# Optimization experiments

Hardware: AMD Instinct MI355X
Metric: run time of the kernel (lower is better)

The kernel has to match this reference:

```python
import jax, jax.numpy as jnp
import numpy as np
from jax import lax

DN = ('NCDHW', 'OIDHW', 'NCDHW')
BN_EPS = 1e-5  # eval-mode BatchNorm3d with running_mean=0, running_var=1


def conv3d(x, w, b):
    y = lax.conv_general_dilated(x, w, window_strides=(1, 1, 1),
                                 padding=[(1, 1)] * 3, dimension_numbers=DN)
    return y + b[None, :, None, None, None]


def maxpool2(x):
    return lax.reduce_window(x, -jnp.inf, lax.max,
                             (1, 1, 2, 2, 2), (1, 1, 2, 2, 2), 'VALID')


def spline_block(x, cw, cb, knots, sw, w1, w2, g, beta):
    # SplineConv3d: conv -> (BSpline3D blend with SiLU) -> BN(eval) -> maxpool
    y = conv3d(x, cw, cb)                                   # [b,c,d,h,w]
    basis = jnp.maximum(y[..., None] - knots, 0.0) ** 3     # [b,c,d,h,w,k]
    sp = jnp.einsum('bcdhwk,ck->bcdhw', basis, sw)
    out = (w1[None, :, None, None, None] * sp
           + w2[None, :, None, None, None] * (y * jax.nn.sigmoid(y)))
    scale = (g / jnp.sqrt(1.0 + BN_EPS))[None, :, None, None, None]
    return maxpool2(out * scale + beta[None, :, None, None, None])


def setup_inputs() -> dict:
    key = jax.random.key(0)
    ks = iter(jax.random.split(key, 40))
    def nrm(shape, s=1.0):
        return jax.random.normal(next(ks), shape, dtype=jnp.float32) * s
    d = {}
    d['x'] = nrm((2, 1, 64, 64, 64))
    for cin, cout, t in [(1, 32, '1'), (32, 64, '2'), (64, 128, '3')]:
        d[f'c{t}_w'] = nrm((cout, cin, 3, 3, 3), 0.1)
        d[f'c{t}_b'] = nrm((cout,), 0.01)
        d[f'c{t}_knots'] = jnp.linspace(-1.0, 1.0, 10).astype(jnp.float32)
        d[f'c{t}_sw'] = nrm((cout, 10), 0.2)
        d[f'c{t}_w1'] = nrm((cout,), 0.2)
        d[f'c{t}_w2'] = nrm((cout,), 0.2)
        d[f'bn{t}_g'] = 1.0 + nrm((cout,), 0.1)
        d[f'bn{t}_b'] = nrm((cout,), 0.1)
    d['fc1_w'] = nrm((256, 128), 0.05)
    d['fc1_b'] = nrm((256,), 0.01)
    d['fc2_w'] = nrm((2, 256), 0.05)
    d['fc2_b'] = nrm((2,), 0.01)
    return d


def reference(x,
              c1_w, c1_b, c1_knots, c1_sw, c1_w1, c1_w2, bn1_g, bn1_b,
              c2_w, c2_b, c2_knots, c2_sw, c2_w1, c2_w2, bn2_g, bn2_b,
              c3_w, c3_b, c3_knots, c3_sw, c3_w1, c3_w2, bn3_g, bn3_b,
              fc1_w, fc1_b, fc2_w, fc2_b):
    h = spline_block(x, c1_w, c1_b, c1_knots, c1_sw, c1_w1, c1_w2, bn1_g, bn1_b)
    h = spline_block(h, c2_w, c2_b, c2_knots, c2_sw, c2_w1, c2_w2, bn2_g, bn2_b)
    h = spline_block(h, c3_w, c3_b, c3_knots, c3_sw, c3_w1, c3_w2, bn3_g, bn3_b)
    h = h.mean(axis=(2, 3, 4))          # AdaptiveAvgPool3d((1,1,1)) + flatten
    h = jax.nn.relu(h @ fc1_w.T + fc1_b)  # dropout is identity in eval mode
    return h @ fc2_w.T + fc2_b
```

## Files before the change

kernel.cpp:

```cpp
#include <hip/hip_runtime.h>
#include <math.h>


#define GLOBAL_AS __attribute__((address_space(1)))
#define LDS_AS    __attribute__((address_space(3)))

static __device__ __forceinline__ void async_ld16(const float* g, float* l) {
    __builtin_amdgcn_global_load_lds((const GLOBAL_AS void*)g, (LDS_AS void*)l,
                                     16, 0, 0);
}

template <int TPB_, int CIN, int CSPLIT, int G,
          int WDT, int WHT, int WWT, int BD, int BH, int BW>
__global__ __launch_bounds__(TPB_, 2) void spline_block_kernel(
    const float* __restrict__ x,
    const float* __restrict__ cw,
    const float* __restrict__ cb,
    const float* __restrict__ knots,
    const float* __restrict__ sw,
    const float* __restrict__ w1,
    const float* __restrict__ w2,
    const float* __restrict__ g,
    const float* __restrict__ beta,
    const float* __restrict__ zbuf,
    float* __restrict__ out,
    int N, int Cout, int D, int H, int W,
    int ntiles, int nthw, int ntw)
{
    constexpr int NSW    = BD * BH * BW;
    constexpr int NW     = TPB_ / 64;
    constexpr int CPG    = CIN / CSPLIT;
    constexpr int ID     = 2 * WDT + 2;
    constexpr int IH     = 2 * WHT + 2;
    constexpr int CHK    = (WWT + 4) / 2;
    constexpr int PITCH  = CHK * 4;
    constexpr int ROWS   = ID * IH;
    constexpr int CHUNKS = ROWS * CHK;
    constexpr int PHYS   = CHUNKS * 4;
    constexpr int NCH    = (CHUNKS + 63) / 64;
    constexpr int BUFS   = (CPG > 1) ? 2 : 1;
    static_assert(NW == NSW * CSPLIT, "waves = spatial-tiles x cin-split");
    static_assert(WDT * WHT * WWT == 64, "one wave per spatial tile");
    static_assert(CIN % CSPLIT == 0, "cin divisible");
    static_assert(NCH <= 32, "mask fits u32");
    static_assert(NCH == 6, "s_waitcnt vmcnt(6) literal assumes 6 issues/cin");
    static_assert(CSPLIT == 1 ||
                  (CSPLIT - 1) * 64 * G * 8 <= NW * BUFS * PHYS,
                  "reduction scratch fits in tile");

    __shared__ __align__(16) float tile[NW][BUFS][PHYS];
    __shared__ float  wlds[CIN * G * 28];
    __shared__ float4 stbl[G * 11];

    const int PD = D >> 1, PH = H >> 1, PW = W >> 1;
    const int groups = Cout / G;
    const int tid  = threadIdx.x;
    const int wv   = tid >> 6;
    const int lane = tid & 63;
    const int sw_  = wv % NSW;
    const int cg   = wv / NSW;

    const int bx      = blockIdx.x;
    const int tile_id = bx % ntiles;
    const int t1      = bx / ntiles;
    const int grp     = t1 % groups;
    const int n       = t1 / groups;
    const int c0      = grp * G;
    const int cinbase = cg * CPG;

    const int td  = tile_id / nthw;
    const int rem = tile_id % nthw;
    const int th_ = rem / ntw;
    const int tw_ = rem % ntw;

    for (int i = tid; i < CIN * G * 27; i += TPB_) {
        const int t  = i % 27;
        const int cgr = i / 27;
        const int gg = cgr % G;
        const int ci = cgr / G;
        wlds[cgr * 28 + t] = cw[((c0 + gg) * CIN + ci) * 27 + t];
    }
    for (int i = tid; i < G * 11; i += TPB_) {
        const int gg  = i / 11;
        const int cnt = i % 11;
        const int c   = c0 + gg;
        float A = 0.f, B3 = 0.f, C3 = 0.f, Dd = 0.f;
        for (int j = 0; j < cnt; j++) {
            const float s = sw[c * 10 + j];
            const float k = knots[j];
            A  += s;
            B3 += 3.0f * s * k;
            C3 += 3.0f * s * k * k;
            Dd += s * k * k * k;
        }
        stbl[i] = make_float4(A, B3, C3, Dd);
    }

    const int swd = sw_ / (BH * BW);
    const int r2  = sw_ % (BH * BW);
    const int swh = r2 / BW;
    const int sww = r2 % BW;
    const int pd0 = td  * (BD * WDT) + swd * WDT;
    const int ph0 = th_ * (BH * WHT) + swh * WHT;
    const int pw0 = tw_ * (BW * WWT) + sww * WWT;

    const int pwl = lane % WWT;
    const int phl = (lane / WWT) % WHT;
    const int pdl = lane / (WWT * WHT);

    const int d0 = 2 * pd0 - 1, h0 = 2 * ph0 - 1;
    const int w0 = 2 * pw0 - 1;
    const int wb = w0 & ~3;
    const int woff = w0 - wb;

    int off[NCH];
    unsigned vm = 0;
#pragma unroll
    for (int k = 0; k < NCH; k++) {
        const int chunk = lane + 64 * k;
        const int row = chunk / CHK, cs = chunk - row * CHK;
        const int dz = row / IH, hy = row - dz * IH;
        const int dd = d0 + dz, hh = h0 + hy;
        const int wsd = wb + cs * 4;
        const bool ok = (chunk < CHUNKS) &
                        ((unsigned)dd < (unsigned)D) &
                        ((unsigned)hh < (unsigned)H) &
                        ((unsigned)wsd < (unsigned)W);
        off[k] = ok ? (dd * H + hh) * W + wsd : 0;
        vm |= (unsigned)ok << k;
    }

    const size_t chstride = (size_t)D * H * W;
    const float* xn = x + (size_t)n * CIN * chstride;

    float acc[G][8];
#pragma unroll
    for (int gg = 0; gg < G; gg++)
#pragma unroll
        for (int i = 0; i < 8; i++) acc[gg][i] = 0.0f;

    __syncthreads();

    auto stage = [&](int ci, int buf) {
        const float* xc = xn + (size_t)ci * chstride;
        float* dst = &tile[wv][buf][0];
#pragma unroll
        for (int k = 0; k < NCH; k++) {
            const int chunk = lane + 64 * k;
            if ((k + 1) * 64 <= CHUNKS || chunk < CHUNKS) {
                const float* src = ((vm >> k) & 1) ? (xc + off[k]) : zbuf;
                async_ld16(src, dst + chunk * 4);
            }
        }
    };

    stage(cinbase, 0);

#pragma unroll 1
    for (int s = 0; s < CPG; s++) {
        const int cur = s & (BUFS - 1);
        if (s + 1 < CPG) {
            stage(cinbase + s + 1, cur ^ 1);
            asm volatile("s_waitcnt vmcnt(6)" ::: "memory");
        } else {
            asm volatile("s_waitcnt vmcnt(0)" ::: "memory");
        }

        const int ci = cinbase + s;
        const float* tb = &tile[wv][cur][0];
        float r[64];
#pragma unroll
        for (int dz = 0; dz < 4; dz++)
#pragma unroll
        for (int dy = 0; dy < 4; dy++) {
            const int rb = ((2 * pdl + dz) * IH + (2 * phl + dy)) * PITCH +
                           woff + 2 * pwl;
            r[(dz * 4 + dy) * 4 + 0] = tb[rb + 0];
            r[(dz * 4 + dy) * 4 + 1] = tb[rb + 1];
            r[(dz * 4 + dy) * 4 + 2] = tb[rb + 2];
            r[(dz * 4 + dy) * 4 + 3] = tb[rb + 3];
        }

#pragma unroll
        for (int gg = 0; gg < G; gg++) {
            const float4* w4p = (const float4*)&wlds[(ci * G + gg) * 28];
#pragma unroll
            for (int ch = 0; ch < 7; ch++) {
                const float4 wv4 = w4p[ch];
#pragma unroll
                for (int j = 0; j < 4; j++) {
                    const int tap = ch * 4 + j;
                    if (tap < 27) {
                        const float wvj = (j == 0) ? wv4.x : (j == 1) ? wv4.y
                                        : (j == 2) ? wv4.z : wv4.w;
                        const int kd = tap / 9, kh = (tap % 9) / 3, kw = tap % 3;
#pragma unroll
                        for (int od = 0; od < 2; od++)
#pragma unroll
                        for (int oh = 0; oh < 2; oh++)
#pragma unroll
                        for (int ow = 0; ow < 2; ow++)
                            acc[gg][(od * 2 + oh) * 2 + ow] =
                                fmaf(wvj,
                                     r[((od + kd) * 4 + (oh + kh)) * 4 + (ow + kw)],
                                     acc[gg][(od * 2 + oh) * 2 + ow]);
                    }
                }
            }
        }
    }

    float* af = &acc[0][0];
    if (CSPLIT > 1) {
        __syncthreads();
        float* scratch = &tile[0][0][0];
        if (cg > 0) {
#pragma unroll
            for (int idx = 0; idx < G * 8; idx++)
                scratch[(idx * (CSPLIT - 1) + (cg - 1)) * 64 + lane] = af[idx];
        }
        __syncthreads();
        if (cg == 0) {
#pragma unroll
            for (int idx = 0; idx < G * 8; idx++) {
                float s2 = af[idx];
                for (int j = 0; j < CSPLIT - 1; j++)
                    s2 += scratch[(idx * (CSPLIT - 1) + j) * 64 + lane];
                af[idx] = s2;
            }
        }
    }

    if (cg == 0) {
        const int pdg = pd0 + pdl, phg = ph0 + phl, pwg = pw0 + pwl;
#pragma unroll
        for (int gg = 0; gg < G; gg++) {
            const int c = c0 + gg;
            const float bias = cb[c];
            const float W1 = w1[c], W2 = w2[c];
            const float scale = g[c] * rsqrtf(1.0f + 1e-5f);
            const float bb = beta[c];

            float m = -INFINITY;
#pragma unroll
            for (int i = 0; i < 8; i++) {
                const float y = acc[gg][i] + bias;
                int idx = (int)floorf((y + 1.0f) * 4.5f) + 1;
                idx = min(max(idx, 0), 10);
                const float4 cf = stbl[gg * 11 + idx];
                const float sp = ((cf.x * y - cf.y) * y + cf.z) * y - cf.w;
                const float silu = y / (1.0f + __expf(-y));
                const float o = fmaf(W1 * sp + W2 * silu, scale, bb);
                m = fmaxf(m, o);
            }
            out[((size_t)(n * Cout + c) * PD + pdg) * PH * PW + phg * PW + pwg] = m;
        }
    }
}

__global__ __launch_bounds__(64) void mean_kernel(
    const float* __restrict__ h, float* __restrict__ out, int S)
{
    const int nc = blockIdx.x;
    const int lane = threadIdx.x;
    const float* p = h + (size_t)nc * S;
    float s = 0.0f;
    for (int i = lane; i < S; i += 64) s += p[i];
#pragma unroll
    for (int off = 32; off > 0; off >>= 1) s += __shfl_down(s, off, 64);
    if (lane == 0) out[nc] = s / (float)S;
}

__global__ __launch_bounds__(256) void fc_kernel(
    const float* __restrict__ pooled,
    const float* __restrict__ w1, const float* __restrict__ b1,
    const float* __restrict__ w2, const float* __restrict__ b2,
    float* __restrict__ out)
{
    __shared__ float hbuf[2][256];
    const int j = threadIdx.x;
#pragma unroll
    for (int nn = 0; nn < 2; nn++) {
        float s = b1[j];
        for (int k = 0; k < 128; k++)
            s = fmaf(pooled[nn * 128 + k], w1[j * 128 + k], s);
        hbuf[nn][j] = fmaxf(s, 0.0f);
    }
    __syncthreads();
    const int wid = j >> 6, lane = j & 63;
    const int nn = wid >> 1, oo = wid & 1;
    float s = 0.0f;
    for (int k = lane; k < 256; k += 64) s += hbuf[nn][k] * w2[oo * 256 + k];
#pragma unroll
    for (int off = 32; off > 0; off >>= 1) s += __shfl_down(s, off, 64);
    if (lane == 0) out[nn * 2 + oo] = s + b2[oo];
}

extern "C" void kernel_launch(void* const* d_in, const int* in_sizes, int n_in,
                              void* d_out, int out_size, void* d_ws, size_t ws_size,
                              hipStream_t stream) {
    const float* x      = (const float*)d_in[0];
    const float* c1_w   = (const float*)d_in[1];
    const float* c1_b   = (const float*)d_in[2];
    const float* c1_kn  = (const float*)d_in[3];
    const float* c1_sw  = (const float*)d_in[4];
    const float* c1_w1  = (const float*)d_in[5];
    const float* c1_w2  = (const float*)d_in[6];
    const float* bn1_g  = (const float*)d_in[7];
    const float* bn1_b  = (const float*)d_in[8];
    const float* c2_w   = (const float*)d_in[9];
    const float* c2_b   = (const float*)d_in[10];
    const float* c2_kn  = (const float*)d_in[11];
    const float* c2_sw  = (const float*)d_in[12];
    const float* c2_w1  = (const float*)d_in[13];
    const float* c2_w2  = (const float*)d_in[14];
    const float* bn2_g  = (const float*)d_in[15];
    const float* bn2_b  = (const float*)d_in[16];
    const float* c3_w   = (const float*)d_in[17];
    const float* c3_b   = (const float*)d_in[18];
    const float* c3_kn  = (const float*)d_in[19];
    const float* c3_sw  = (const float*)d_in[20];
    const float* c3_w1  = (const float*)d_in[21];
    const float* c3_w2  = (const float*)d_in[22];
    const float* bn3_g  = (const float*)d_in[23];
    const float* bn3_b  = (const float*)d_in[24];
    const float* fc1_w  = (const float*)d_in[25];
    const float* fc1_b  = (const float*)d_in[26];
    const float* fc2_w  = (const float*)d_in[27];
    const float* fc2_b  = (const float*)d_in[28];

    float* ws = (float*)d_ws;
    float* h1     = ws;
    float* h2     = h1 + 2097152;
    float* h3     = h2 + 524288;
    float* pooled = h3 + 131072;
    float* zbuf   = pooled + 256;

    hipMemsetAsync(zbuf, 0, 64, stream);

    spline_block_kernel<256, 1, 1, 4, 2, 4, 8, 2, 2, 1>
        <<<dim3(2048), dim3(256), 0, stream>>>(
        x, c1_w, c1_b, c1_kn, c1_sw, c1_w1, c1_w2, bn1_g, bn1_b, zbuf, h1,
        2, 32, 64, 64, 64, 128, 16, 4);
    spline_block_kernel<256, 32, 1, 4, 2, 4, 8, 2, 2, 1>
        <<<dim3(512), dim3(256), 0, stream>>>(
        h1, c2_w, c2_b, c2_kn, c2_sw, c2_w1, c2_w2, bn2_g, bn2_b, zbuf, h2,
        2, 64, 32, 32, 32, 16, 4, 2);
    spline_block_kernel<256, 64, 4, 4, 2, 4, 8, 1, 1, 1>
        <<<dim3(512), dim3(256), 0, stream>>>(
        h2, c3_w, c3_b, c3_kn, c3_sw, c3_w1, c3_w2, bn3_g, bn3_b, zbuf, h3,
        2, 128, 16, 16, 16, 8, 2, 1);
    mean_kernel<<<dim3(256), dim3(64), 0, stream>>>(h3, pooled, 512);
    fc_kernel<<<dim3(1), dim3(256), 0, stream>>>(pooled, fc1_w, fc1_b, fc2_w, fc2_b,
                                                 (float*)d_out);
}
```

Measured before the change: 324.8 us.

## Repack conv weights to padded float4 in global and read directly, drop LDS staging

Adds a repack kernel that copies each layer's 27-tap conv weights into 28-float padded rows. Each spline block now reads those rows as wave-uniform float4 global loads instead of staging the weights in LDS at block start. This frees the LDS weight buffer and removes the per-block staging loop. Layer 2 also changes its tiling to a 2-way cin split with 1x1x2 spatial tiles and twice as many blocks. The cost is an extra kernel launch and weight reads on the inner loop that depend on the cache.

```diff
diff --git a/kernel.cpp b/kernel.cpp
--- a/kernel.cpp
+++ b/kernel.cpp
@@ -8,13 +8,30 @@
 static __device__ __forceinline__ void async_ld16(const float* g, float* l) {
     __builtin_amdgcn_global_load_lds((const GLOBAL_AS void*)g, (LDS_AS void*)l,
                                      16, 0, 0);
+}
+
+__global__ __launch_bounds__(256) void repack_kernel(
+    const float* __restrict__ w1, const float* __restrict__ w2,
+    const float* __restrict__ w3,
+    float* __restrict__ o1, float* __restrict__ o2, float* __restrict__ o3)
+{
+    const int i = blockIdx.x * 256 + threadIdx.x;
+    const float* src;
+    float* dst;
+    if (i < 32)            { src = w1 + i * 27;           dst = o1 + i * 28; }
+    else if (i < 2080)     { const int j = i - 32;   src = w2 + j * 27; dst = o2 + j * 28; }
+    else if (i < 10272)    { const int j = i - 2080; src = w3 + j * 27; dst = o3 + j * 28; }
+    else return;
+#pragma unroll
+    for (int t = 0; t < 27; t++) dst[t] = src[t];
+    dst[27] = 0.0f;
 }
 
 template <int TPB_, int CIN, int CSPLIT, int G,
           int WDT, int WHT, int WWT, int BD, int BH, int BW>
 __global__ __launch_bounds__(TPB_, 2) void spline_block_kernel(
     const float* __restrict__ x,
-    const float* __restrict__ cw,
+    const float4* __restrict__ wpk,
     const float* __restrict__ cb,
     const float* __restrict__ knots,
     const float* __restrict__ sw,
@@ -49,7 +66,6 @@
                   "reduction scratch fits in tile");
 
     __shared__ __align__(16) float tile[NW][BUFS][PHYS];
-    __shared__ float  wlds[CIN * G * 28];
     __shared__ float4 stbl[G * 11];
 
     const int PD = D >> 1, PH = H >> 1, PW = W >> 1;
@@ -73,13 +89,6 @@
     const int th_ = rem / ntw;
     const int tw_ = rem % ntw;
 
-    for (int i = tid; i < CIN * G * 27; i += TPB_) {
-        const int t  = i % 27;
-        const int cgr = i / 27;
-        const int gg = cgr % G;
-        const int ci = cgr / G;
-        wlds[cgr * 28 + t] = cw[((c0 + gg) * CIN + ci) * 27 + t];
-    }
     for (int i = tid; i < G * 11; i += TPB_) {
         const int gg  = i / 11;
         const int cnt = i % 11;
@@ -183,16 +192,18 @@
 
 #pragma unroll
         for (int gg = 0; gg < G; gg++) {
-            const float4* w4p = (const float4*)&wlds[(ci * G + gg) * 28];
+            const float4* wp = wpk + ((size_t)(c0 + gg) * CIN + ci) * 7;
+            float4 q[7];
+#pragma unroll
+            for (int ch = 0; ch < 7; ch++) q[ch] = wp[ch];
 #pragma unroll
             for (int ch = 0; ch < 7; ch++) {
-                const float4 wv4 = w4p[ch];
 #pragma unroll
                 for (int j = 0; j < 4; j++) {
                     const int tap = ch * 4 + j;
                     if (tap < 27) {
-                        const float wvj = (j == 0) ? wv4.x : (j == 1) ? wv4.y
-                                        : (j == 2) ? wv4.z : wv4.w;
+                        const float wvj = (j == 0) ? q[ch].x : (j == 1) ? q[ch].y
+                                        : (j == 2) ? q[ch].z : q[ch].w;
                         const int kd = tap / 9, kh = (tap % 9) / 3, kw = tap % 3;
 #pragma unroll
                         for (int od = 0; od < 2; od++)
@@ -335,21 +346,27 @@
     float* h3     = h2 + 524288;
     float* pooled = h3 + 131072;
     float* zbuf   = pooled + 256;
+    float* wp1    = zbuf + 16;
+    float* wp2    = wp1 + 896;
+    float* wp3    = wp2 + 57344;
 
     hipMemsetAsync(zbuf, 0, 64, stream);
+
+    repack_kernel<<<dim3(41), dim3(256), 0, stream>>>(c1_w, c2_w, c3_w,
+                                                      wp1, wp2, wp3);
 
     spline_block_kernel<256, 1, 1, 4, 2, 4, 8, 2, 2, 1>
         <<<dim3(2048), dim3(256), 0, stream>>>(
-        x, c1_w, c1_b, c1_kn, c1_sw, c1_w1, c1_w2, bn1_g, bn1_b, zbuf, h1,
-        2, 32, 64, 64, 64, 128, 16, 4);
-    spline_block_kernel<256, 32, 1, 4, 2, 4, 8, 2, 2, 1>
-        <<<dim3(512), dim3(256), 0, stream>>>(
-        h1, c2_w, c2_b, c2_kn, c2_sw, c2_w1, c2_w2, bn2_g, bn2_b, zbuf, h2,
-        2, 64, 32, 32, 32, 16, 4, 2);
+        x, (const float4*)wp1, c1_b, c1_kn, c1_sw, c1_w1, c1_w2, bn1_g, bn1_b,
+        zbuf, h1, 2, 32, 64, 64, 64, 128, 16, 4);
+    spline_block_kernel<256, 32, 2, 4, 2, 4, 8, 1, 1, 2>
+        <<<dim3(1024), dim3(256), 0, stream>>>(
+        h1, (const float4*)wp2, c2_b, c2_kn, c2_sw, c2_w1, c2_w2, bn2_g, bn2_b,
+        zbuf, h2, 2, 64, 32, 32, 32, 32, 4, 1);
     spline_block_kernel<256, 64, 4, 4, 2, 4, 8, 1, 1, 1>
         <<<dim3(512), dim3(256), 0, stream>>>(
-        h2, c3_w, c3_b, c3_kn, c3_sw, c3_w1, c3_w2, bn3_g, bn3_b, zbuf, h3,
-        2, 128, 16, 16, 16, 8, 2, 1);
+        h2, (const float4*)wp3, c3_b, c3_kn, c3_sw, c3_w1, c3_w2, bn3_g, bn3_b,
+        zbuf, h3, 2, 128, 16, 16, 16, 8, 2, 1);
     mean_kernel<<<dim3(256), dim3(64), 0, stream>>>(h3, pooled, 512);
     fc_kernel<<<dim3(1), dim3(256), 0, stream>>>(pooled, fc1_w, fc1_b, fc2_w, fc2_b,
                                                  (float*)d_out);
```

Result: no change. 327.8 us (+0.9%).
